# Performance work log

Measured on AMD Instinct MI355X. Metric: run time of the kernel, lower is better.

## Reference

```python
import jax, jax.numpy as jnp
import numpy as np

N, IN_DIM, HID, H1, NCLS, H2, E = 50000, 256, 32, 8, 16, 8, 800000


def gat_conv(x, edge_index, W, a_src, a_dst, b, H, C):
    """PyG-style GATConv, eval mode (attention dropout off), concat=True,
    negative_slope=0.2, add_self_loops=True."""
    n = x.shape[0]
    loop = jnp.arange(n)
    src = jnp.concatenate([edge_index[0], loop])  # [E+N]
    dst = jnp.concatenate([edge_index[1], loop])
    h = (x @ W).reshape(n, H, C)                  # [N,H,C]
    alpha_s = jnp.sum(h * a_src, axis=-1)         # [N,H]
    alpha_d = jnp.sum(h * a_dst, axis=-1)         # [N,H]
    e = jax.nn.leaky_relu(alpha_s[src] + alpha_d[dst], 0.2)  # [E+N,H]
    # segment softmax over incoming edges of each target node
    e_max = jax.ops.segment_max(e, dst, num_segments=n)      # [N,H] (self-loop guarantees nonempty)
    p = jnp.exp(e - e_max[dst])
    denom = jax.ops.segment_sum(p, dst, num_segments=n)
    alpha = p / (denom[dst] + 1e-16)              # [E+N,H]
    msg = h[src] * alpha[:, :, None]              # [E+N,H,C]
    out = jax.ops.segment_sum(msg, dst, num_segments=n)      # [N,H,C]
    return out.reshape(n, H * C) + b


def setup_inputs() -> dict:
    key = jax.random.key(0)
    ks = jax.random.split(key, 12)
    x = jax.random.normal(ks[0], (N, IN_DIM), dtype=jnp.float32)
    edge_index = jax.random.randint(ks[1], (2, E), 0, N, dtype=jnp.int64)
    s1 = 1.0 / np.sqrt(IN_DIM)
    s2 = 1.0 / np.sqrt(HID * H1)
    W1 = jax.random.normal(ks[2], (IN_DIM, H1 * HID), dtype=jnp.float32) * s1
    a_src1 = jax.random.normal(ks[3], (H1, HID), dtype=jnp.float32) * s1
    a_dst1 = jax.random.normal(ks[4], (H1, HID), dtype=jnp.float32) * s1
    b1 = jnp.zeros((H1 * HID,), dtype=jnp.float32)
    W2 = jax.random.normal(ks[5], (H1 * HID, H2 * NCLS), dtype=jnp.float32) * s2
    a_src2 = jax.random.normal(ks[6], (H2, NCLS), dtype=jnp.float32) * s2
    a_dst2 = jax.random.normal(ks[7], (H2, NCLS), dtype=jnp.float32) * s2
    b2 = jnp.zeros((H2 * NCLS,), dtype=jnp.float32)
    return {"x": x, "edge_index": edge_index, "W1": W1, "a_src1": a_src1,
            "a_dst1": a_dst1, "b1": b1, "W2": W2, "a_src2": a_src2,
            "a_dst2": a_dst2, "b2": b2}


def reference(x, edge_index, W1, a_src1, a_dst1, b1, W2, a_src2, a_dst2, b2):
    # eval mode: F.dropout is identity
    h = gat_conv(x, edge_index, W1, a_src1, a_dst1, b1, H1, HID)   # [N, H1*HID]
    h = jax.nn.elu(h)
    h = gat_conv(h, edge_index, W2, a_src2, a_dst2, b2, H2, NCLS)  # [N, H2*NCLS]
    return jax.nn.log_softmax(h, axis=1)
```

## Files before the change

### kernel.cpp

```cpp
#include <hip/hip_runtime.h>
#include <hip/hip_fp16.h>

#define NN 50000
#define NE 800000

typedef _Float16 half4v __attribute__((ext_vector_type(4)));
typedef _Float16 half8v __attribute__((ext_vector_type(8)));
typedef float f32x4 __attribute__((ext_vector_type(4)));

#define Q_SCALE 0.04724409448f
#define Q_INV   21.16666667f

static __device__ __forceinline__ float lrelu(float x) { return x > 0.f ? x : 0.2f * x; }

__global__ void detect_i64_kernel(const unsigned* __restrict__ ei, int* __restrict__ flag) {
  if (threadIdx.x == 0 && blockIdx.x == 0) {
    int is64 = 1;
    for (int i = 0; i < 64; ++i)
      if (ei[2 * i + 1] != 0u) { is64 = 0; break; }
    *flag = is64;
  }
}

static __device__ __forceinline__ int edge_at(const void* ei, int is64, long long idx) {
  if (is64) return (int)((const long long*)ei)[idx];
  return ((const int*)ei)[idx];
}

__global__ void count_kernel(const void* __restrict__ ei, const int* __restrict__ flag,
                             int* __restrict__ counts) {
  int e = blockIdx.x * blockDim.x + threadIdx.x;
  if (e >= NE) return;
  int is64 = *flag;
  int d = edge_at(ei, is64, (long long)NE + e);
  atomicAdd(&counts[d], 1);
}

static __device__ __forceinline__ int block_scan_inc(int v, int tid) {
  __shared__ int ws[4];
  const int lane = tid & 63, wv = tid >> 6;
  #pragma unroll
  for (int off = 1; off < 64; off <<= 1) {
    int t = __shfl_up(v, off);
    if (lane >= off) v += t;
  }
  if (lane == 63) ws[wv] = v;
  __syncthreads();
  int add = 0;
  #pragma unroll
  for (int j = 0; j < 4; ++j) if (j < wv) add += ws[j];
  return v + add;
}

__global__ void scan1_kernel(const int* __restrict__ counts, int* __restrict__ bsums) {
  __shared__ int ws[4];
  const int tid = threadIdx.x;
  const int lane = tid & 63, wv = tid >> 6;
  int i = blockIdx.x * 256 + tid;
  int v = (i < NN) ? counts[i] : 0;
  #pragma unroll
  for (int off = 1; off < 64; off <<= 1) v += __shfl_xor(v, off);
  if (lane == 0) ws[wv] = v;
  __syncthreads();
  if (tid == 0) bsums[blockIdx.x] = ws[0] + ws[1] + ws[2] + ws[3];
}

__global__ void scan2_kernel(int* __restrict__ bsums, int nb) {
  const int tid = threadIdx.x;
  int v = (tid < nb) ? bsums[tid] : 0;
  int inc = block_scan_inc(v, tid);
  if (tid < nb) bsums[tid] = inc - v;
}

__global__ void scan3_kernel(const int* __restrict__ counts, const int* __restrict__ bsums,
                             int* __restrict__ rs) {
  const int tid = threadIdx.x;
  int i = blockIdx.x * 256 + tid;
  int v = (i < NN) ? counts[i] : 0;
  int inc = block_scan_inc(v, tid);
  if (i < NN) rs[i + 1] = bsums[blockIdx.x] + inc;
  if (i == 0) rs[0] = 0;
}

__global__ void scatter_kernel(const void* __restrict__ ei, const int* __restrict__ flag,
                               const int* __restrict__ rs, int* __restrict__ cursor,
                               int* __restrict__ ssrc) {
  int e = blockIdx.x * blockDim.x + threadIdx.x;
  if (e >= NE) return;
  int is64 = *flag;
  int s = edge_at(ei, is64, e);
  int d = edge_at(ei, is64, (long long)NE + e);
  int p = atomicAdd(&cursor[d], 1);
  ssrc[rs[d] + p] = s;
}

__global__ void prep_kernel(const float* __restrict__ W1, const float* __restrict__ W2,
                            const float* __restrict__ aS1, const float* __restrict__ aD1,
                            const float* __restrict__ aS2, const float* __restrict__ aD2,
                            _Float16* __restrict__ W1t, _Float16* __restrict__ W2t,
                            _Float16* __restrict__ Wa1, _Float16* __restrict__ Wa2) {
  int i = blockIdx.x * blockDim.x + threadIdx.x;
  if (i < 65536) {
    int n = i >> 8, k = i & 255;
    W1t[i] = (_Float16)W1[(size_t)k * 256 + n];
  } else if (i < 98304) {
    int j = i - 65536;
    int n = j >> 8, k = j & 255;
    W2t[j] = (_Float16)W2[(size_t)k * 128 + n];
  } else if (i < 102400) {
    int j = i - 98304;
    int row = j >> 8, k = j & 255;
    int head = row & 7;
    const float* a = (row < 8) ? aS1 : aD1;
    float s = 0.f;
    #pragma unroll 8
    for (int c = 0; c < 32; ++c)
      s += W1[(size_t)k * 256 + head * 32 + c] * a[head * 32 + c];
    Wa1[j] = (_Float16)s;
  } else if (i < 106496) {
    int j = i - 102400;
    int row = j >> 8, k = j & 255;
    int head = row & 7;
    const float* a = (row < 8) ? aS2 : aD2;
    float s = 0.f;
    #pragma unroll 8
    for (int c = 0; c < 16; ++c)
      s += W2[(size_t)k * 128 + head * 16 + c] * a[head * 16 + c];
    Wa2[j] = (_Float16)s;
  }
}

template<int BN, int NCF, bool A_HALF, bool Q8OUT>
__global__ __launch_bounds__(256) void gemm_mfma(const void* __restrict__ Araw,
                                                 const _Float16* __restrict__ Wt,
                                                 const _Float16* __restrict__ Wa,
                                                 void* __restrict__ Cout,
                                                 float* __restrict__ alS,
                                                 float* __restrict__ alD, int M) {
  __shared__ __align__(16) _Float16 As[64][256 + 8];
  const int tid = threadIdx.x;
  const int bm0 = blockIdx.x * 64;
  if (A_HALF) {
    const _Float16* A = (const _Float16*)Araw;
    for (int idx = tid; idx < 64 * 32; idx += 256) {
      int r = idx >> 5, c8 = (idx & 31) << 3;
      int gr = bm0 + r;
      half8v v = {};
      if (gr < M) v = *(const half8v*)&A[(size_t)gr * 256 + c8];
      *(half8v*)&As[r][c8] = v;
    }
  } else {
    const float* A = (const float*)Araw;
    for (int idx = tid; idx < 64 * 64; idx += 256) {
      int r = idx >> 6, c4 = (idx & 63) << 2;
      int gr = bm0 + r;
      float4 v = make_float4(0.f, 0.f, 0.f, 0.f);
      if (gr < M) v = *(const float4*)&A[(size_t)gr * 256 + c4];
      half4v h = { (_Float16)v.x, (_Float16)v.y, (_Float16)v.z, (_Float16)v.w };
      *(half4v*)&As[r][c4] = h;
    }
  }
  __syncthreads();
  const int lane = tid & 63, wv = tid >> 6;
  const int ncol0 = wv * (16 * NCF);
  const int lrow = lane & 15, lk8 = (lane >> 4) << 3;
  f32x4 acc[4][NCF];
  f32x4 acca[4];
  #pragma unroll
  for (int rf = 0; rf < 4; ++rf) {
    acca[rf] = (f32x4){0.f, 0.f, 0.f, 0.f};
    #pragma unroll
    for (int cf = 0; cf < NCF; ++cf) acc[rf][cf] = (f32x4){0.f, 0.f, 0.f, 0.f};
  }
  #pragma unroll
  for (int k0 = 0; k0 < 256; k0 += 32) {
    const int ks = k0 + lk8;
    half8v af[4];
    #pragma unroll
    for (int rf = 0; rf < 4; ++rf)
      af[rf] = *(const half8v*)&As[16 * rf + lrow][ks];
    #pragma unroll
    for (int cf = 0; cf < NCF; ++cf) {
      half8v bf = *(const half8v*)&Wt[(size_t)(ncol0 + 16 * cf + lrow) * 256 + ks];
      #pragma unroll
      for (int rf = 0; rf < 4; ++rf)
        acc[rf][cf] = __builtin_amdgcn_mfma_f32_16x16x32_f16(af[rf], bf, acc[rf][cf], 0, 0, 0);
    }
    if (wv == 0) {
      half8v bfa = *(const half8v*)&Wa[(size_t)lrow * 256 + ks];
      #pragma unroll
      for (int rf = 0; rf < 4; ++rf)
        acca[rf] = __builtin_amdgcn_mfma_f32_16x16x32_f16(af[rf], bfa, acca[rf], 0, 0, 0);
    }
  }
  if (Q8OUT) {
    __syncthreads();
    char* Cs = (char*)&As[0][0];
    #pragma unroll
    for (int rf = 0; rf < 4; ++rf) {
      #pragma unroll
      for (int j = 0; j < 4; ++j) {
        int r = 16 * rf + 4 * (lane >> 4) + j;
        #pragma unroll
        for (int cf = 0; cf < NCF; ++cf) {
          int col = ncol0 + 16 * cf + lrow;
          float v = acc[rf][cf][j];
          int q = __float2int_rn(fminf(fmaxf(v * Q_INV, -127.f), 127.f)) + 128;
          Cs[r * 256 + col] = (char)q;
        }
      }
    }
    __syncthreads();
    unsigned char* C8 = (unsigned char*)Cout;
    for (int idx = tid; idx < 64 * 16; idx += 256) {
      int r = idx >> 4, c16 = idx & 15;
      int grow = bm0 + r;
      if (grow < M)
        *(int4*)&C8[(size_t)grow * 256 + 16 * c16] = *(const int4*)&Cs[r * 256 + 16 * c16];
    }
  } else {
    __half* C = (__half*)Cout;
    #pragma unroll
    for (int rf = 0; rf < 4; ++rf) {
      #pragma unroll
      for (int j = 0; j < 4; ++j) {
        int row = bm0 + 16 * rf + 4 * (lane >> 4) + j;
        if (row < M) {
          #pragma unroll
          for (int cf = 0; cf < NCF; ++cf) {
            int col = ncol0 + 16 * cf + lrow;
            C[(size_t)row * BN + col] = __float2half(acc[rf][cf][j]);
          }
        }
      }
    }
  }
  if (wv == 0) {
    #pragma unroll
    for (int rf = 0; rf < 4; ++rf) {
      #pragma unroll
      for (int j = 0; j < 4; ++j) {
        int row = bm0 + 16 * rf + 4 * (lane >> 4) + j;
        if (row < M) {
          float v = acca[rf][j];
          if (lrow < 8) alS[row * 8 + lrow] = v;
          else          alD[row * 8 + (lrow - 8)] = v;
        }
      }
    }
  }
}

#define ACCQ(w, p) do { \
    ax0 += (p) * (float)((w) & 255u); \
    ax1 += (p) * (float)(((w) >> 8) & 255u); \
    ax2 += (p) * (float)(((w) >> 16) & 255u); \
    ax3 += (p) * (float)((w) >> 24); \
  } while (0)

__global__ __launch_bounds__(256) void agg1_kernel(const unsigned char* __restrict__ h1q,
    const float* __restrict__ as, const float* __restrict__ ad,
    const int* __restrict__ rs, const int* __restrict__ ssrc,
    const float* __restrict__ bias, __half* __restrict__ out) {
  const int wid = (blockIdx.x * blockDim.x + threadIdx.x) >> 6;
  const int lane = threadIdx.x & 63;
  if (wid >= NN) return;
  const int node = wid;
  const int beg = rs[node], end = rs[node + 1];
  const int deg = end - beg;
  const int hd = lane >> 3;
  const float advh = ad[node * 8 + hd];
  const unsigned* hw = (const unsigned*)h1q;
  float denom = 0.f;
  float ax0 = 0.f, ax1 = 0.f, ax2 = 0.f, ax3 = 0.f;
  {
    float p = __expf(lrelu(as[node * 8 + hd] + advh));
    unsigned w = hw[(size_t)node * 64 + lane];
    ACCQ(w, p);
    denom = p;
  }
  for (int base = 0; base < deg; base += 64) {
    const int cnt = min(deg - base, 64);
    int sv = (lane < cnt) ? ssrc[beg + base + lane] : 0;
    int j = 0;
    for (; j + 8 <= cnt; j += 8) {
      int s0 = __builtin_amdgcn_readlane(sv, j + 0);
      int s1 = __builtin_amdgcn_readlane(sv, j + 1);
      int s2 = __builtin_amdgcn_readlane(sv, j + 2);
      int s3 = __builtin_amdgcn_readlane(sv, j + 3);
      int s4 = __builtin_amdgcn_readlane(sv, j + 4);
      int s5 = __builtin_amdgcn_readlane(sv, j + 5);
      int s6 = __builtin_amdgcn_readlane(sv, j + 6);
      int s7 = __builtin_amdgcn_readlane(sv, j + 7);
      float b0 = as[s0 * 8 + hd], b1 = as[s1 * 8 + hd];
      float b2 = as[s2 * 8 + hd], b3 = as[s3 * 8 + hd];
      float b4 = as[s4 * 8 + hd], b5 = as[s5 * 8 + hd];
      float b6 = as[s6 * 8 + hd], b7 = as[s7 * 8 + hd];
      unsigned w0 = hw[(size_t)s0 * 64 + lane];
      unsigned w1 = hw[(size_t)s1 * 64 + lane];
      unsigned w2 = hw[(size_t)s2 * 64 + lane];
      unsigned w3 = hw[(size_t)s3 * 64 + lane];
      unsigned w4 = hw[(size_t)s4 * 64 + lane];
      unsigned w5 = hw[(size_t)s5 * 64 + lane];
      unsigned w6 = hw[(size_t)s6 * 64 + lane];
      unsigned w7 = hw[(size_t)s7 * 64 + lane];
      float p0 = __expf(lrelu(b0 + advh)), p1 = __expf(lrelu(b1 + advh));
      float p2 = __expf(lrelu(b2 + advh)), p3 = __expf(lrelu(b3 + advh));
      float p4 = __expf(lrelu(b4 + advh)), p5 = __expf(lrelu(b5 + advh));
      float p6 = __expf(lrelu(b6 + advh)), p7 = __expf(lrelu(b7 + advh));
      denom += (p0 + p1) + (p2 + p3) + ((p4 + p5) + (p6 + p7));
      ACCQ(w0, p0); ACCQ(w1, p1); ACCQ(w2, p2); ACCQ(w3, p3);
      ACCQ(w4, p4); ACCQ(w5, p5); ACCQ(w6, p6); ACCQ(w7, p7);
    }
    for (; j < cnt; ++j) {
      int s = __builtin_amdgcn_readlane(sv, j);
      float p = __expf(lrelu(as[s * 8 + hd] + advh));
      unsigned w = hw[(size_t)s * 64 + lane];
      ACCQ(w, p);
      denom += p;
    }
  }
  const float inv = 1.f / (denom + 1e-16f);
  const float4 bv = *(const float4*)&bias[lane * 4];
  float4 o;
  o.x = Q_SCALE * (ax0 * inv - 128.f) + bv.x;
  o.y = Q_SCALE * (ax1 * inv - 128.f) + bv.y;
  o.z = Q_SCALE * (ax2 * inv - 128.f) + bv.z;
  o.w = Q_SCALE * (ax3 * inv - 128.f) + bv.w;
  o.x = o.x > 0.f ? o.x : __expf(o.x) - 1.f;
  o.y = o.y > 0.f ? o.y : __expf(o.y) - 1.f;
  o.z = o.z > 0.f ? o.z : __expf(o.z) - 1.f;
  o.w = o.w > 0.f ? o.w : __expf(o.w) - 1.f;
  union { __half2 h2[2]; float2 f2; } w;
  w.h2[0] = __floats2half2_rn(o.x, o.y);
  w.h2[1] = __floats2half2_rn(o.z, o.w);
  *(float2*)&out[(size_t)node * 256 + lane * 4] = w.f2;
}

__global__ __launch_bounds__(256) void agg2_kernel(const __half* __restrict__ h,
    const float* __restrict__ as, const float* __restrict__ ad,
    const int* __restrict__ rs, const int* __restrict__ ssrc,
    const float* __restrict__ bias, float* __restrict__ out) {
  const int wid = (blockIdx.x * blockDim.x + threadIdx.x) >> 6;
  const int lane = threadIdx.x & 63;
  if (wid >= NN) return;
  const int node = wid;
  const int beg = rs[node], end = rs[node + 1];
  const int deg = end - beg;
  const int hd = lane >> 3;
  const float advh = ad[node * 8 + hd];
  float denom;
  __half2 acc;
  {
    float p = __expf(lrelu(as[node * 8 + hd] + advh));
    __half2 q = ((const __half2*)&h[(size_t)node * 128])[lane];
    acc = __hmul2(__float2half2_rn(p), q);
    denom = p;
  }
  for (int base = 0; base < deg; base += 64) {
    const int cnt = min(deg - base, 64);
    int sv = (lane < cnt) ? ssrc[beg + base + lane] : 0;
    int j = 0;
    for (; j + 8 <= cnt; j += 8) {
      int s0 = __builtin_amdgcn_readlane(sv, j + 0);
      int s1 = __builtin_amdgcn_readlane(sv, j + 1);
      int s2 = __builtin_amdgcn_readlane(sv, j + 2);
      int s3 = __builtin_amdgcn_readlane(sv, j + 3);
      int s4 = __builtin_amdgcn_readlane(sv, j + 4);
      int s5 = __builtin_amdgcn_readlane(sv, j + 5);
      int s6 = __builtin_amdgcn_readlane(sv, j + 6);
      int s7 = __builtin_amdgcn_readlane(sv, j + 7);
      float b0 = as[s0 * 8 + hd], b1 = as[s1 * 8 + hd];
      float b2 = as[s2 * 8 + hd], b3 = as[s3 * 8 + hd];
      float b4 = as[s4 * 8 + hd], b5 = as[s5 * 8 + hd];
      float b6 = as[s6 * 8 + hd], b7 = as[s7 * 8 + hd];
      __half2 q0 = ((const __half2*)&h[(size_t)s0 * 128])[lane];
      __half2 q1 = ((const __half2*)&h[(size_t)s1 * 128])[lane];
      __half2 q2 = ((const __half2*)&h[(size_t)s2 * 128])[lane];
      __half2 q3 = ((const __half2*)&h[(size_t)s3 * 128])[lane];
      __half2 q4 = ((const __half2*)&h[(size_t)s4 * 128])[lane];
      __half2 q5 = ((const __half2*)&h[(size_t)s5 * 128])[lane];
      __half2 q6 = ((const __half2*)&h[(size_t)s6 * 128])[lane];
      __half2 q7 = ((const __half2*)&h[(size_t)s7 * 128])[lane];
      float p0 = __expf(lrelu(b0 + advh)), p1 = __expf(lrelu(b1 + advh));
      float p2 = __expf(lrelu(b2 + advh)), p3 = __expf(lrelu(b3 + advh));
      float p4 = __expf(lrelu(b4 + advh)), p5 = __expf(lrelu(b5 + advh));
      float p6 = __expf(lrelu(b6 + advh)), p7 = __expf(lrelu(b7 + advh));
      denom += (p0 + p1) + (p2 + p3) + ((p4 + p5) + (p6 + p7));
      acc = __hfma2(__float2half2_rn(p0), q0, acc);
      acc = __hfma2(__float2half2_rn(p1), q1, acc);
      acc = __hfma2(__float2half2_rn(p2), q2, acc);
      acc = __hfma2(__float2half2_rn(p3), q3, acc);
      acc = __hfma2(__float2half2_rn(p4), q4, acc);
      acc = __hfma2(__float2half2_rn(p5), q5, acc);
      acc = __hfma2(__float2half2_rn(p6), q6, acc);
      acc = __hfma2(__float2half2_rn(p7), q7, acc);
    }
    for (; j < cnt; ++j) {
      int s = __builtin_amdgcn_readlane(sv, j);
      float p = __expf(lrelu(as[s * 8 + hd] + advh));
      __half2 q = ((const __half2*)&h[(size_t)s * 128])[lane];
      acc = __hfma2(__float2half2_rn(p), q, acc);
      denom += p;
    }
  }
  const float inv = 1.f / (denom + 1e-16f);
  float2 av = __half22float2(acc);
  float v0 = av.x * inv + bias[lane * 2 + 0];
  float v1 = av.y * inv + bias[lane * 2 + 1];
  float mx = fmaxf(v0, v1);
  #pragma unroll
  for (int off = 1; off < 64; off <<= 1) mx = fmaxf(mx, __shfl_xor(mx, off));
  float sum = __expf(v0 - mx) + __expf(v1 - mx);
  #pragma unroll
  for (int off = 1; off < 64; off <<= 1) sum += __shfl_xor(sum, off);
  float lse = mx + __logf(sum);
  float2 o = make_float2(v0 - lse, v1 - lse);
  __builtin_nontemporal_store(o.x, &out[(size_t)node * 128 + lane * 2]);
  __builtin_nontemporal_store(o.y, &out[(size_t)node * 128 + lane * 2 + 1]);
}

extern "C" void kernel_launch(void* const* d_in, const int* in_sizes, int n_in,
                              void* d_out, int out_size, void* d_ws, size_t ws_size,
                              hipStream_t stream) {
  const float* x    = (const float*)d_in[0];
  const void*  ei   = d_in[1];
  const float* W1   = (const float*)d_in[2];
  const float* aS1  = (const float*)d_in[3];
  const float* aD1  = (const float*)d_in[4];
  const float* b1   = (const float*)d_in[5];
  const float* W2   = (const float*)d_in[6];
  const float* aS2  = (const float*)d_in[7];
  const float* aD2  = (const float*)d_in[8];
  const float* b2   = (const float*)d_in[9];
  float* out = (float*)d_out;

  char* ws = (char*)d_ws;
  unsigned char* h1q = (unsigned char*)ws; ws += (size_t)NN * 256;
  __half* h2   = (__half*)ws;          ws += (size_t)NN * 128 * 2;
  __half* hmid = (__half*)ws;          ws += (size_t)NN * 256 * 2;
  _Float16* W1t = (_Float16*)ws;       ws += (size_t)256 * 256 * 2;
  _Float16* W2t = (_Float16*)ws;       ws += (size_t)128 * 256 * 2;
  _Float16* Wa1 = (_Float16*)ws;       ws += (size_t)16 * 256 * 2;
  _Float16* Wa2 = (_Float16*)ws;       ws += (size_t)16 * 256 * 2;
  float* alS  = (float*)ws;            ws += (size_t)NN * 8 * 4;
  float* alD  = (float*)ws;            ws += (size_t)NN * 8 * 4;
  int* counts = (int*)ws;              ws += (size_t)NN * 4;
  int* rs     = (int*)ws;              ws += (size_t)(NN + 1) * 4;
  int* bsums  = (int*)ws;              ws += (size_t)256 * 4;
  int* ssrc   = (int*)ws;              ws += (size_t)NE * 4;
  int* flag   = (int*)ws;              ws += 256;

  const int NB = (NN + 255) / 256;

  detect_i64_kernel<<<1, 64, 0, stream>>>((const unsigned*)ei, flag);
  hipMemsetAsync(counts, 0, (size_t)NN * 4, stream);
  count_kernel<<<(NE + 255) / 256, 256, 0, stream>>>(ei, flag, counts);
  scan1_kernel<<<NB, 256, 0, stream>>>(counts, bsums);
  scan2_kernel<<<1, 256, 0, stream>>>(bsums, NB);
  scan3_kernel<<<NB, 256, 0, stream>>>(counts, bsums, rs);
  hipMemsetAsync(counts, 0, (size_t)NN * 4, stream);
  scatter_kernel<<<(NE + 255) / 256, 256, 0, stream>>>(ei, flag, rs, counts, ssrc);

  prep_kernel<<<(106496 + 255) / 256, 256, 0, stream>>>(W1, W2, aS1, aD1, aS2, aD2,
                                                        W1t, W2t, Wa1, Wa2);

  const int ngrid = (NN + 63) / 64;
  gemm_mfma<256, 4, false, true><<<ngrid, 256, 0, stream>>>(x, W1t, Wa1, h1q, alS, alD, NN);
  agg1_kernel<<<(NN + 3) / 4, 256, 0, stream>>>(h1q, alS, alD, rs, ssrc, b1, hmid);

  gemm_mfma<128, 2, true, false><<<ngrid, 256, 0, stream>>>(hmid, W2t, Wa2, h2, alS, alD, NN);
  agg2_kernel<<<(NN + 3) / 4, 256, 0, stream>>>(h2, alS, alD, rs, ssrc, b2, out);
}
```

Baseline: 240.1 us.

## Pre-pack weights into MFMA fragment order and use 512-thread GEMM blocks

```diff
diff --git a/kernel.cpp b/kernel.cpp
--- a/kernel.cpp
+++ b/kernel.cpp
@@ -97,43 +97,51 @@
 __global__ void prep_kernel(const float* __restrict__ W1, const float* __restrict__ W2,
                             const float* __restrict__ aS1, const float* __restrict__ aD1,
                             const float* __restrict__ aS2, const float* __restrict__ aD2,
-                            _Float16* __restrict__ W1t, _Float16* __restrict__ W2t,
-                            _Float16* __restrict__ Wa1, _Float16* __restrict__ Wa2) {
+                            _Float16* __restrict__ W1p, _Float16* __restrict__ W2p,
+                            _Float16* __restrict__ Wa1p, _Float16* __restrict__ Wa2p) {
   int i = blockIdx.x * blockDim.x + threadIdx.x;
   if (i < 65536) {
-    int n = i >> 8, k = i & 255;
-    W1t[i] = (_Float16)W1[(size_t)k * 256 + n];
+    int j = i & 7, l = (i >> 3) & 63, kst = (i >> 9) & 7, ct = i >> 12;
+    int col = ct * 16 + (l & 15);
+    int k = kst * 32 + ((l >> 4) << 3) + j;
+    W1p[i] = (_Float16)W1[(size_t)k * 256 + col];
   } else if (i < 98304) {
-    int j = i - 65536;
-    int n = j >> 8, k = j & 255;
-    W2t[j] = (_Float16)W2[(size_t)k * 128 + n];
+    int n = i - 65536;
+    int j = n & 7, l = (n >> 3) & 63, kst = (n >> 9) & 7, ct = n >> 12;
+    int col = ct * 16 + (l & 15);
+    int k = kst * 32 + ((l >> 4) << 3) + j;
+    W2p[n] = (_Float16)W2[(size_t)k * 128 + col];
   } else if (i < 102400) {
-    int j = i - 98304;
-    int row = j >> 8, k = j & 255;
+    int n = i - 98304;
+    int j = n & 7, l = (n >> 3) & 63, kst = n >> 9;
+    int row = l & 15;
     int head = row & 7;
     const float* a = (row < 8) ? aS1 : aD1;
+    int k = kst * 32 + ((l >> 4) << 3) + j;
     float s = 0.f;
     #pragma unroll 8
     for (int c = 0; c < 32; ++c)
       s += W1[(size_t)k * 256 + head * 32 + c] * a[head * 32 + c];
-    Wa1[j] = (_Float16)s;
+    Wa1p[n] = (_Float16)s;
   } else if (i < 106496) {
-    int j = i - 102400;
-    int row = j >> 8, k = j & 255;
+    int n = i - 102400;
+    int j = n & 7, l = (n >> 3) & 63, kst = n >> 9;
+    int row = l & 15;
     int head = row & 7;
     const float* a = (row < 8) ? aS2 : aD2;
+    int k = kst * 32 + ((l >> 4) << 3) + j;
     float s = 0.f;
     #pragma unroll 8
     for (int c = 0; c < 16; ++c)
       s += W2[(size_t)k * 128 + head * 16 + c] * a[head * 16 + c];
-    Wa2[j] = (_Float16)s;
+    Wa2p[n] = (_Float16)s;
   }
 }
 
 template<int BN, int NCF, bool A_HALF, bool Q8OUT>
-__global__ __launch_bounds__(256) void gemm_mfma(const void* __restrict__ Araw,
-                                                 const _Float16* __restrict__ Wt,
-                                                 const _Float16* __restrict__ Wa,
+__global__ __launch_bounds__(512) void gemm_mfma(const void* __restrict__ Araw,
+                                                 const _Float16* __restrict__ Bp,
+                                                 const _Float16* __restrict__ Wap,
                                                  void* __restrict__ Cout,
                                                  float* __restrict__ alS,
                                                  float* __restrict__ alD, int M) {
@@ -142,22 +150,39 @@
   const int bm0 = blockIdx.x * 64;
   if (A_HALF) {
     const _Float16* A = (const _Float16*)Araw;
-    for (int idx = tid; idx < 64 * 32; idx += 256) {
+    half8v tmp[4]; int rr[4], cc[4];
+    #pragma unroll
+    for (int t = 0; t < 4; ++t) {
+      int idx = tid + t * 512;
       int r = idx >> 5, c8 = (idx & 31) << 3;
       int gr = bm0 + r;
-      half8v v = {};
-      if (gr < M) v = *(const half8v*)&A[(size_t)gr * 256 + c8];
-      *(half8v*)&As[r][c8] = v;
-    }
+      tmp[t] = (half8v){};
+      if (gr < M) tmp[t] = *(const half8v*)&A[(size_t)gr * 256 + c8];
+      rr[t] = r; cc[t] = c8;
+    }
+    #pragma unroll
+    for (int t = 0; t < 4; ++t)
+      *(half8v*)&As[rr[t]][cc[t]] = tmp[t];
   } else {
     const float* A = (const float*)Araw;
-    for (int idx = tid; idx < 64 * 64; idx += 256) {
-      int r = idx >> 6, c4 = (idx & 63) << 2;
-      int gr = bm0 + r;
-      float4 v = make_float4(0.f, 0.f, 0.f, 0.f);
-      if (gr < M) v = *(const float4*)&A[(size_t)gr * 256 + c4];
-      half4v h = { (_Float16)v.x, (_Float16)v.y, (_Float16)v.z, (_Float16)v.w };
-      *(half4v*)&As[r][c4] = h;
+    #pragma unroll
+    for (int g = 0; g < 2; ++g) {
+      float4 tmp[4]; int rr[4], cc[4];
+      #pragma unroll
+      for (int t = 0; t < 4; ++t) {
+        int idx = tid + (g * 4 + t) * 512;
+        int r = idx >> 6, c4 = (idx & 63) << 2;
+        int gr = bm0 + r;
+        tmp[t] = make_float4(0.f, 0.f, 0.f, 0.f);
+        if (gr < M) tmp[t] = *(const float4*)&A[(size_t)gr * 256 + c4];
+        rr[t] = r; cc[t] = c4;
+      }
+      #pragma unroll
+      for (int t = 0; t < 4; ++t) {
+        half4v h = { (_Float16)tmp[t].x, (_Float16)tmp[t].y,
+                     (_Float16)tmp[t].z, (_Float16)tmp[t].w };
+        *(half4v*)&As[rr[t]][cc[t]] = h;
+      }
     }
   }
   __syncthreads();
@@ -173,21 +198,21 @@
     for (int cf = 0; cf < NCF; ++cf) acc[rf][cf] = (f32x4){0.f, 0.f, 0.f, 0.f};
   }
   #pragma unroll
-  for (int k0 = 0; k0 < 256; k0 += 32) {
-    const int ks = k0 + lk8;
+  for (int kst = 0; kst < 8; ++kst) {
+    const int ks = kst * 32 + lk8;
     half8v af[4];
     #pragma unroll
     for (int rf = 0; rf < 4; ++rf)
       af[rf] = *(const half8v*)&As[16 * rf + lrow][ks];
     #pragma unroll
     for (int cf = 0; cf < NCF; ++cf) {
-      half8v bf = *(const half8v*)&Wt[(size_t)(ncol0 + 16 * cf + lrow) * 256 + ks];
+      half8v bf = *(const half8v*)&Bp[((size_t)((wv * NCF + cf) * 8 + kst) * 64 + lane) * 8];
       #pragma unroll
       for (int rf = 0; rf < 4; ++rf)
         acc[rf][cf] = __builtin_amdgcn_mfma_f32_16x16x32_f16(af[rf], bf, acc[rf][cf], 0, 0, 0);
     }
     if (wv == 0) {
-      half8v bfa = *(const half8v*)&Wa[(size_t)lrow * 256 + ks];
+      half8v bfa = *(const half8v*)&Wap[((size_t)kst * 64 + lane) * 8];
       #pragma unroll
       for (int rf = 0; rf < 4; ++rf)
         acca[rf] = __builtin_amdgcn_mfma_f32_16x16x32_f16(af[rf], bfa, acca[rf], 0, 0, 0);
@@ -200,23 +225,25 @@
     for (int rf = 0; rf < 4; ++rf) {
       #pragma unroll
       for (int j = 0; j < 4; ++j) {
-        int r = 16 * rf + 4 * (lane >> 4) + j;
+        int r = 16 * rf + 4 * ((lane >> 4) & 3) + j;
         #pragma unroll
         for (int cf = 0; cf < NCF; ++cf) {
           int col = ncol0 + 16 * cf + lrow;
           float v = acc[rf][cf][j];
           int q = __float2int_rn(fminf(fmaxf(v * Q_INV, -127.f), 127.f)) + 128;
-          Cs[r * 256 + col] = (char)q;
+          Cs[r * 272 + col] = (char)q;
         }
       }
     }
     __syncthreads();
     unsigned char* C8 = (unsigned char*)Cout;
-    for (int idx = tid; idx < 64 * 16; idx += 256) {
+    #pragma unroll
+    for (int g = 0; g < 2; ++g) {
+      int idx = tid + g * 512;
       int r = idx >> 4, c16 = idx & 15;
       int grow = bm0 + r;
       if (grow < M)
-        *(int4*)&C8[(size_t)grow * 256 + 16 * c16] = *(const int4*)&Cs[r * 256 + 16 * c16];
+        *(int4*)&C8[(size_t)grow * 256 + 16 * c16] = *(const int4*)&Cs[r * 272 + 16 * c16];
     }
   } else {
     __half* C = (__half*)Cout;
@@ -224,7 +251,7 @@
     for (int rf = 0; rf < 4; ++rf) {
       #pragma unroll
       for (int j = 0; j < 4; ++j) {
-        int row = bm0 + 16 * rf + 4 * (lane >> 4) + j;
+        int row = bm0 + 16 * rf + 4 * ((lane >> 4) & 3) + j;
         if (row < M) {
           #pragma unroll
           for (int cf = 0; cf < NCF; ++cf) {
@@ -240,7 +267,7 @@
     for (int rf = 0; rf < 4; ++rf) {
       #pragma unroll
       for (int j = 0; j < 4; ++j) {
-        int row = bm0 + 16 * rf + 4 * (lane >> 4) + j;
+        int row = bm0 + 16 * rf + 4 * ((lane >> 4) & 3) + j;
         if (row < M) {
           float v = acca[rf][j];
           if (lrow < 8) alS[row * 8 + lrow] = v;
@@ -439,10 +466,10 @@
   unsigned char* h1q = (unsigned char*)ws; ws += (size_t)NN * 256;
   __half* h2   = (__half*)ws;          ws += (size_t)NN * 128 * 2;
   __half* hmid = (__half*)ws;          ws += (size_t)NN * 256 * 2;
-  _Float16* W1t = (_Float16*)ws;       ws += (size_t)256 * 256 * 2;
-  _Float16* W2t = (_Float16*)ws;       ws += (size_t)128 * 256 * 2;
-  _Float16* Wa1 = (_Float16*)ws;       ws += (size_t)16 * 256 * 2;
-  _Float16* Wa2 = (_Float16*)ws;       ws += (size_t)16 * 256 * 2;
+  _Float16* W1p = (_Float16*)ws;       ws += (size_t)65536 * 2;
+  _Float16* W2p = (_Float16*)ws;       ws += (size_t)32768 * 2;
+  _Float16* Wa1p = (_Float16*)ws;      ws += (size_t)4096 * 2;
+  _Float16* Wa2p = (_Float16*)ws;      ws += (size_t)4096 * 2;
   float* alS  = (float*)ws;            ws += (size_t)NN * 8 * 4;
   float* alD  = (float*)ws;            ws += (size_t)NN * 8 * 4;
   int* counts = (int*)ws;              ws += (size_t)NN * 4;
@@ -463,12 +490,12 @@
   scatter_kernel<<<(NE + 255) / 256, 256, 0, stream>>>(ei, flag, rs, counts, ssrc);
 
   prep_kernel<<<(106496 + 255) / 256, 256, 0, stream>>>(W1, W2, aS1, aD1, aS2, aD2,
-                                                        W1t, W2t, Wa1, Wa2);
+                                                        W1p, W2p, Wa1p, Wa2p);
 
   const int ngrid = (NN + 63) / 64;
-  gemm_mfma<256, 4, false, true><<<ngrid, 256, 0, stream>>>(x, W1t, Wa1, h1q, alS, alD, NN);
+  gemm_mfma<256, 2, false, true><<<ngrid, 512, 0, stream>>>(x, W1p, Wa1p, h1q, alS, alD, NN);
   agg1_kernel<<<(NN + 3) / 4, 256, 0, stream>>>(h1q, alS, alD, rs, ssrc, b1, hmid);
 
-  gemm_mfma<128, 2, true, false><<<ngrid, 256, 0, stream>>>(hmid, W2t, Wa2, h2, alS, alD, NN);
+  gemm_mfma<128, 1, true, false><<<ngrid, 512, 0, stream>>>(hmid, W2p, Wa2p, h2, alS, alD, NN);
   agg2_kernel<<<(NN + 3) / 4, 256, 0, stream>>>(h2, alS, alD, rs, ssrc, b2, out);
 }
```

Measured after the change: 220.8 us. 8.1% less time.
